# Kernel optimization log

Measured on AMD Instinct MI355X. Metric: run time of the kernel, lower is better.

The kernel has to match this reference:

```python
import jax, jax.numpy as jnp
import numpy as np

B, T, D, H, K, V, W = 2, 2048, 768, 12, 64, 64, 1024
EPS = 1e-6


def setup_inputs() -> dict:
    key = jax.random.key(0)
    ks = jax.random.split(key, 10)
    std = 0.02
    return {
        "x": jax.random.normal(ks[0], (B, T, D), jnp.float32),
        "gdn_state": jax.random.normal(ks[1], (B, H, K, V), jnp.float32),
        "Wq": jax.random.normal(ks[2], (D, H * K), jnp.float32) * std,
        "Wk": jax.random.normal(ks[3], (D, H * K), jnp.float32) * std,
        "Wv": jax.random.normal(ks[4], (D, H * K), jnp.float32) * std,
        "Wo": jax.random.normal(ks[5], (H * K, D), jnp.float32) * std,
        "Wgq": jax.random.normal(ks[6], (D, H * K), jnp.float32) * std,
        "Wro": jax.random.normal(ks[7], (H * V, D), jnp.float32) * std,
        "Wg": jax.random.normal(ks[8], (D, H), jnp.float32) * std,
        "bg": jnp.full((H,), 1.0, jnp.float32),  # swa_gate_init
        "norm_w": jnp.ones((D,), jnp.float32),
    }


def reference(x, gdn_state, Wq, Wk, Wv, Wo, Wgq, Wro, Wg, bg, norm_w):
    # RMSNorm
    xn = x * jax.lax.rsqrt(jnp.mean(x * x, axis=-1, keepdims=True) + EPS) * norm_w

    def proj(w):  # (B,T,D)@(D,HK) -> (B,H,T,K)
        return (xn @ w).reshape(B, T, H, K).transpose(0, 2, 1, 3)

    q, k, v = proj(Wq), proj(Wk), proj(Wv)
    scale = K ** -0.5

    scores = jnp.einsum("bhqk,bhsk->bhqs", q, k) * scale  # (B,H,T,T)
    i = jnp.arange(T)[:, None]
    j = jnp.arange(T)[None, :]
    allowed = (j <= i) & (j >= i - W)  # causal sliding window
    scores = jnp.where(allowed, scores, -jnp.inf)
    attn = jax.nn.softmax(scores, axis=-1)

    local = jnp.einsum("bhqs,bhsk->bhqk", attn, v)
    local = local.transpose(0, 2, 1, 3).reshape(B, T, H * K) @ Wo  # (B,T,D)

    # GDN state retrieval
    qg = jax.nn.relu((xn @ Wgq).reshape(B, T, H, K).transpose(0, 2, 1, 3))  # (B,H,T,K)
    retrieved = jnp.einsum("bhkv,bhtk->bhtv", gdn_state, qg)  # (B,H,T,V)
    retrieval = retrieved.transpose(0, 2, 1, 3).reshape(B, T, H * V) @ Wro  # (B,T,D)
    gate = jax.nn.sigmoid(xn @ Wg + bg)  # (B,T,H)
    retrieval = jnp.mean(gate, axis=-1, keepdims=True) * retrieval

    return x + local + retrieval
```

## Files before the change

kernel.cpp:

```cpp
#include <hip/hip_runtime.h>
#include <math.h>
#include <stdint.h>

typedef float f32x4 __attribute__((ext_vector_type(4)));
typedef __bf16 bf16x8 __attribute__((ext_vector_type(8)));
typedef __bf16 bf16x4 __attribute__((ext_vector_type(4)));

constexpr int Bc = 2, Tc = 2048, Dc = 768, Hc = 12, Wc = 1024;
#define CEXP 0.18033688011112042f

__device__ __forceinline__ f32x4 mfma_bf16(bf16x8 a, bf16x8 b, f32x4 c) {
    return __builtin_amdgcn_mfma_f32_16x16x32_bf16(a, b, c, 0, 0, 0);
}
__device__ __forceinline__ void gload16(const void* g, void* l) {
    __builtin_amdgcn_global_load_lds(
        (const __attribute__((address_space(1))) uint32_t*)g,
        (__attribute__((address_space(3))) uint32_t*)l, 16, 0, 0);
}
__device__ __forceinline__ uint32_t pack2(float a, float b) {
    union { __bf16 h[2]; uint32_t u; } x;
    x.h[0] = (__bf16)a; x.h[1] = (__bf16)b; return x.u;
}
__device__ __forceinline__ void s_wait_vm8()   { asm volatile("s_waitcnt vmcnt(8)" ::: "memory"); }
__device__ __forceinline__ void s_wait_vm4()   { asm volatile("s_waitcnt vmcnt(4)" ::: "memory"); }
__device__ __forceinline__ void s_wait_vm0()   { asm volatile("s_waitcnt vmcnt(0)" ::: "memory"); }
__device__ __forceinline__ void s_wait_lgkm0() { asm volatile("s_waitcnt lgkmcnt(0)" ::: "memory"); }
__device__ __forceinline__ void bar()          { __builtin_amdgcn_s_barrier(); }
__device__ __forceinline__ void wait_tiles(int infl) {
    if (infl >= 2) s_wait_vm8();
    else if (infl == 1) s_wait_vm4();
    else s_wait_vm0();
}

__global__ __launch_bounds__(256) void k_prep_w(
    const float* __restrict__ Wq, const float* __restrict__ Wk,
    const float* __restrict__ Wv, const float* __restrict__ Wgq,
    const float* __restrict__ Wo, const float* __restrict__ Wro,
    __bf16* __restrict__ wTproj, __bf16* __restrict__ wTout)
{
    __shared__ __bf16 ldsT[64][66];
    const int wsel = blockIdx.y;
    const float* srcs[6] = {Wq, Wk, Wv, Wgq, Wo, Wro};
    const float* src = srcs[wsel];
    __bf16* dst; int dstride, koff;
    if (wsel < 4) { dst = wTproj + (size_t)wsel * Dc * Dc; dstride = Dc;  koff = 0; }
    else if (wsel == 4) { dst = wTout; dstride = 1536; koff = 0; }
    else { dst = wTout; dstride = 1536; koff = 768; }
    const float scale = (wsel == 0) ? CEXP : 1.0f;

    int tile = blockIdx.x;
    int tk = tile % 12, tn = tile / 12;
    int k0 = tk * 64, n0 = tn * 64;
    int i = threadIdx.x, rsub = i >> 4, c4 = i & 15;
#pragma unroll
    for (int rep = 0; rep < 4; ++rep) {
        int row = rep * 16 + rsub;
        float4 v = *(const float4*)(src + (size_t)(k0 + row) * Dc + n0 + c4 * 4);
        ldsT[c4 * 4 + 0][row] = (__bf16)(v.x * scale);
        ldsT[c4 * 4 + 1][row] = (__bf16)(v.y * scale);
        ldsT[c4 * 4 + 2][row] = (__bf16)(v.z * scale);
        ldsT[c4 * 4 + 3][row] = (__bf16)(v.w * scale);
    }
    __syncthreads();
#pragma unroll
    for (int rep = 0; rep < 4; ++rep) {
        int n = rep * 16 + rsub;
        bf16x4 o = *(const bf16x4*)&ldsT[n][c4 * 4];
        *(bf16x4*)(dst + (size_t)(n0 + n) * dstride + koff + k0 + c4 * 4) = o;
    }
}

__global__ __launch_bounds__(256) void k_prep_state(
    const float* __restrict__ st, __bf16* __restrict__ stT)
{
    int idx = blockIdx.x * 256 + threadIdx.x;
    int bh = idx >> 12, kk = (idx >> 6) & 63, vv = idx & 63;
    stT[(size_t)bh * 4096 + vv * 64 + kk] = (__bf16)st[idx];
}

__global__ __launch_bounds__(256) void k_prep_wgt(
    const float* __restrict__ Wg, float* __restrict__ WgT)
{
    int i = blockIdx.x * 256 + threadIdx.x;
    int h = i / Dc, d = i - h * Dc;
    WgT[i] = Wg[d * 12 + h];
}

__global__ __launch_bounds__(256) void k_rmsnorm(
    const float* __restrict__ x, const float* __restrict__ norm_w,
    __bf16* __restrict__ xnb)
{
    int row = blockIdx.x, tid = threadIdx.x;
    const float* xr = x + (size_t)row * Dc;
    float4 v = make_float4(0.f, 0.f, 0.f, 0.f);
    float ss = 0.f;
    if (tid < 192) {
        v = ((const float4*)xr)[tid];
        ss = v.x * v.x + v.y * v.y + v.z * v.z + v.w * v.w;
    }
#pragma unroll
    for (int m = 32; m; m >>= 1) ss += __shfl_xor(ss, m, 64);
    __shared__ float red[4];
    if ((tid & 63) == 0) red[tid >> 6] = ss;
    __syncthreads();
    float tot = red[0] + red[1] + red[2] + red[3];
    float rms = rsqrtf(tot * (1.f / 768.f) + 1e-6f);
    if (tid < 192) {
        float4 nw = ((const float4*)norm_w)[tid];
        bf16x4 o;
        o[0] = (__bf16)(v.x * rms * nw.x);
        o[1] = (__bf16)(v.y * rms * nw.y);
        o[2] = (__bf16)(v.z * rms * nw.z);
        o[3] = (__bf16)(v.w * rms * nw.w);
        *(bf16x4*)(xnb + (size_t)row * Dc + tid * 4) = o;
    }
}

__global__ __launch_bounds__(256) void k_gate(
    const __bf16* __restrict__ xnb, const float* __restrict__ WgT,
    const float* __restrict__ bg, float* __restrict__ gmean)
{
    int row = blockIdx.x * 4 + (threadIdx.x >> 6);
    int lane = threadIdx.x & 63;
    const __bf16* xr = xnb + (size_t)row * Dc;
    float p[12];
#pragma unroll
    for (int h = 0; h < 12; ++h) p[h] = 0.f;
    for (int d = lane; d < Dc; d += 64) {
        float xv = (float)xr[d];
#pragma unroll
        for (int h = 0; h < 12; ++h) p[h] += xv * WgT[h * Dc + d];
    }
#pragma unroll
    for (int h = 0; h < 12; ++h) {
#pragma unroll
        for (int m = 32; m; m >>= 1) p[h] += __shfl_xor(p[h], m, 64);
    }
    if (lane == 0) {
        float s = 0.f;
#pragma unroll
        for (int h = 0; h < 12; ++h) s += 1.f / (1.f + expf(-(p[h] + bg[h])));
        gmean[row] = s * (1.f / 12.f);
    }
}

template <int MODE>
__global__ __launch_bounds__(256) void k_gemm(
    const __bf16* __restrict__ A, const __bf16* __restrict__ BT,
    const float* __restrict__ xres, float* __restrict__ outf,
    __bf16* __restrict__ qb, __bf16* __restrict__ kbf,
    __bf16* __restrict__ vtb, __bf16* __restrict__ qgb)
{
    constexpr int BM = (MODE == 0) ? 128 : 64;
    constexpr int BN = (MODE == 0) ? 128 : 64;
    constexpr int KD = (MODE == 0) ? 768 : 1536;
    constexpr int BK = (MODE == 0) ? 32 : 64;
    constexpr int KI = BK / 32;
    constexpr int WM = BM / 2, WN = BN / 2;
    constexpr int MI = WM / 16, NI = WN / 16;
    constexpr int MT = 4096 / BM;
    constexpr int NK = KD / BK;
    constexpr int GR = BK / 8;
    constexpr int ACH = BM * BK / 2048;
    constexpr int BCH = BN * BK / 2048;
    __shared__ __bf16 As[3][BM * BK];
    __shared__ __bf16 Bs[3][BN * BK];
    const int tid = threadIdx.x, w = tid >> 6, lane = tid & 63;
    const int g = lane >> 4, t = lane & 15;
    int id = blockIdx.x, xcd = id & 7, l = id >> 3;
    int nid = xcd * 96 + l;
    int m0 = (nid % MT) * BM, n0 = (nid / MT) * BN;
    const __bf16* Abase = A + (size_t)m0 * KD;
    const __bf16* Bbase = BT + (size_t)n0 * KD;
    const int wrow = (w >> 1) * WM, wcol = (w & 1) * WN;

    auto STAGE = [&](int buf, int k0) {
#pragma unroll
        for (int c = 0; c < ACH; ++c) {
            int chunk = c * 256 + tid, row = chunk / GR, cix = chunk % GR;
            gload16(Abase + (size_t)row * KD + k0 + cix * 8, &As[buf][chunk * 8]);
        }
#pragma unroll
        for (int c = 0; c < BCH; ++c) {
            int chunk = c * 256 + tid, row = chunk / GR, cix = chunk % GR;
            gload16(Bbase + (size_t)row * KD + k0 + cix * 8, &Bs[buf][chunk * 8]);
        }
    };

    f32x4 acc[MI][NI] = {};
    STAGE(0, 0);
    STAGE(1, BK);
    STAGE(2, 2 * BK);
    int buf = 0;
    for (int ks = 0; ks < NK; ++ks) {
        wait_tiles(NK - 1 - ks);
        bar();
        const __bf16* Ab = As[buf];
        const __bf16* Bb = Bs[buf];
        bf16x8 af[MI][KI], bfr[NI][KI];
#pragma unroll
        for (int kk = 0; kk < KI; ++kk) {
#pragma unroll
            for (int mi = 0; mi < MI; ++mi)
                af[mi][kk] = *(const bf16x8*)(Ab + (wrow + mi * 16 + t) * BK + kk * 32 + g * 8);
#pragma unroll
            for (int ni = 0; ni < NI; ++ni)
                bfr[ni][kk] = *(const bf16x8*)(Bb + (wcol + ni * 16 + t) * BK + kk * 32 + g * 8);
        }
        s_wait_lgkm0();
        __builtin_amdgcn_sched_barrier(0);
        bar();
        if (ks + 3 < NK) STAGE(buf, (ks + 3) * BK);
        buf = (buf == 2) ? 0 : buf + 1;
        __builtin_amdgcn_s_setprio(1);
#pragma unroll
        for (int kk = 0; kk < KI; ++kk)
#pragma unroll
            for (int mi = 0; mi < MI; ++mi)
#pragma unroll
                for (int ni = 0; ni < NI; ++ni)
                    acc[mi][ni] = mfma_bf16(af[mi][kk], bfr[ni][kk], acc[mi][ni]);
        __builtin_amdgcn_s_setprio(0);
    }
    const int region = (MODE == 0) ? (n0 / 768) : 0;
#pragma unroll
    for (int mi = 0; mi < MI; ++mi)
#pragma unroll
        for (int ni = 0; ni < NI; ++ni)
#pragma unroll
            for (int r = 0; r < 4; ++r) {
                int grow = m0 + wrow + mi * 16 + g * 4 + r;
                int gcol = n0 + wcol + ni * 16 + t;
                float v = acc[mi][ni][r];
                if (MODE == 1) {
                    size_t idx = (size_t)grow * Dc + gcol;
                    outf[idx] = xres[idx] + v;
                } else {
                    int c = gcol - region * 768;
                    int h = c >> 6, kd = c & 63;
                    int b = grow >> 11, ti = grow & (Tc - 1);
                    if (region == 0)
                        qb[((size_t)(b * Hc + h) * Tc + ti) * 64 + kd] = (__bf16)v;
                    else if (region == 1) {
                        int kds = kd ^ ((ti & 7) << 3);
                        kbf[((size_t)(b * Hc + h) * Tc + ti) * 64 + kds] = (__bf16)v;
                    } else if (region == 2) {
                        int kap = ti & 63;
                        int rho = (kap & 32) | (((kap >> 2) & 3) << 3) |
                                  (((kap >> 4) & 1) << 2) | (kap & 3);
                        int ts = (ti & ~63) | (rho ^ ((kd & 7) << 3));
                        vtb[((size_t)(b * Hc + h) * 64 + kd) * Tc + ts] = (__bf16)v;
                    } else
                        qgb[((size_t)(b * Hc + h) * Tc + ti) * 64 + kd] = (__bf16)fmaxf(v, 0.f);
                }
            }
}

__global__ __launch_bounds__(256) void k_attn(
    const __bf16* __restrict__ q, const __bf16* __restrict__ k,
    const __bf16* __restrict__ vt, __bf16* __restrict__ ac)
{
    __shared__ __bf16 Ks[3][64 * 64];
    __shared__ __bf16 Vs[3][64 * 64];
    int id = blockIdx.x, xcd = id & 7, l = id >> 3;
    int nid = xcd * 96 + l;
    int sblk = nid & 31, h = (nid >> 5) % Hc, b = nid / (32 * Hc);
    int tid = threadIdx.x;
    int w = tid >> 6, lane = tid & 63;
    int g = lane >> 4, t = lane & 15;
    int q0 = sblk * 64, qw = q0 + w * 16;
    const __bf16* qb = q + (size_t)(b * Hc + h) * Tc * 64;
    const __bf16* kb = k + (size_t)(b * Hc + h) * Tc * 64;
    const __bf16* vb = vt + (size_t)(b * Hc + h) * 64 * Tc;

    bf16x8 qf0 = *(const bf16x8*)(qb + (size_t)(qw + t) * 64 + g * 8);
    bf16x8 qf1 = *(const bf16x8*)(qb + (size_t)(qw + t) * 64 + 32 + g * 8);

    const int qi = qw + t;
    const int lowB = qi - Wc;
    const int xr = t & 7;

    f32x4 oacc[4] = {};
    float lsum = 0.f;

    const int s_begin = (q0 >= Wc) ? q0 - Wc : 0;
    const int NT = (q0 + 64 - s_begin) >> 6;

    auto STAGE = [&](int buf, int s0) {
#pragma unroll
        for (int j = 0; j < 2; ++j) {
            int ch = j * 256 + tid;
            gload16(kb + (size_t)(s0 + (ch >> 3)) * 64 + (ch & 7) * 8,
                    &Ks[buf][ch * 8]);
            gload16(vb + (size_t)(ch >> 3) * Tc + s0 + (ch & 7) * 8,
                    &Vs[buf][ch * 8]);
        }
    };

    STAGE(0, s_begin);
    if (NT > 1) STAGE(1, s_begin + 64);
    if (NT > 2) STAGE(2, s_begin + 128);
    int buf = 0;
    for (int it = 0; it < NT; ++it) {
        int s0 = s_begin + it * 64;
        wait_tiles(NT - 1 - it);
        bar();
        const __bf16* Kt = Ks[buf];
        const __bf16* Vt = Vs[buf];
        f32x4 sc[4];
        __builtin_amdgcn_s_setprio(1);
#pragma unroll
        for (int sub = 0; sub < 4; ++sub) {
            const __bf16* kr = Kt + (sub * 16 + t) * 64;
            bf16x8 kA = *(const bf16x8*)(kr + ((g ^ xr) << 3));
            bf16x8 kB = *(const bf16x8*)(kr + (((g + 4) ^ xr) << 3));
            f32x4 s = {};
            s = mfma_bf16(kA, qf0, s);
            s = mfma_bf16(kB, qf1, s);
            sc[sub] = s;
        }
        __builtin_amdgcn_s_setprio(0);
        float pv[4][4];
#pragma unroll
        for (int sub = 0; sub < 4; ++sub)
#pragma unroll
            for (int r = 0; r < 4; ++r) {
                int kk = s0 + sub * 16 + g * 4 + r;
                float e = exp2f(sc[sub][r]);
                float val = (kk <= qi && kk >= lowB) ? e : 0.f;
                pv[sub][r] = val;
                lsum += val;
            }
        __builtin_amdgcn_s_setprio(1);
#pragma unroll
        for (int ks = 0; ks < 2; ++ks) {
            union { uint32_t u[4]; bf16x8 v; } pf;
            pf.u[0] = pack2(pv[ks * 2][0], pv[ks * 2][1]);
            pf.u[1] = pack2(pv[ks * 2][2], pv[ks * 2][3]);
            pf.u[2] = pack2(pv[ks * 2 + 1][0], pv[ks * 2 + 1][1]);
            pf.u[3] = pack2(pv[ks * 2 + 1][2], pv[ks * 2 + 1][3]);
#pragma unroll
            for (int n = 0; n < 4; ++n) {
                const __bf16* vrow = Vt + (n * 16 + t) * 64;
                bf16x8 vf = *(const bf16x8*)(vrow + ((((ks * 4) + g) ^ xr) << 3));
                oacc[n] = mfma_bf16(pf.v, vf, oacc[n]);
            }
        }
        __builtin_amdgcn_s_setprio(0);
        s_wait_lgkm0();
        __builtin_amdgcn_sched_barrier(0);
        bar();
        if (it + 3 < NT) STAGE(buf, s0 + 192);
        buf = (buf == 2) ? 0 : buf + 1;
    }
    lsum += __shfl_xor(lsum, 16, 64);
    lsum += __shfl_xor(lsum, 32, 64);
    float linv = 1.f / lsum;
    float lq[4];
#pragma unroll
    for (int r = 0; r < 4; ++r) lq[r] = __shfl(linv, g * 4 + r, 64);
#pragma unroll
    for (int n = 0; n < 4; ++n)
#pragma unroll
        for (int r = 0; r < 4; ++r) {
            int qrow = qw + g * 4 + r;
            ac[(size_t)(b * Tc + qrow) * 1536 + h * 64 + n * 16 + t] =
                (__bf16)(oacc[n][r] * lq[r]);
        }
}

__global__ __launch_bounds__(256) void k_retr(
    const __bf16* __restrict__ qg, const __bf16* __restrict__ stateT,
    const float* __restrict__ gmean, __bf16* __restrict__ ac)
{
    int b = blockIdx.z, h = blockIdx.y;
    int w = threadIdx.x >> 6, lane = threadIdx.x & 63;
    int g = lane >> 4, t = lane & 15;
    int t0 = blockIdx.x * 64 + w * 16;
    const __bf16* qbp = qg + (size_t)(b * Hc + h) * Tc * 64;
    const __bf16* sb = stateT + (size_t)(b * Hc + h) * 64 * 64;
    bf16x8 a0 = *(const bf16x8*)(qbp + (size_t)(t0 + t) * 64 + g * 8);
    bf16x8 a1 = *(const bf16x8*)(qbp + (size_t)(t0 + t) * 64 + 32 + g * 8);
#pragma unroll
    for (int n = 0; n < 4; ++n) {
        bf16x8 b0 = *(const bf16x8*)(sb + (n * 16 + t) * 64 + g * 8);
        bf16x8 b1 = *(const bf16x8*)(sb + (n * 16 + t) * 64 + 32 + g * 8);
        f32x4 acc = {};
        acc = mfma_bf16(a0, b0, acc);
        acc = mfma_bf16(a1, b1, acc);
#pragma unroll
        for (int r = 0; r < 4; ++r) {
            int ti = t0 + g * 4 + r;
            float gm = gmean[b * Tc + ti];
            ac[(size_t)(b * Tc + ti) * 1536 + 768 + h * 64 + n * 16 + t] =
                (__bf16)(acc[r] * gm);
        }
    }
}

extern "C" void kernel_launch(void* const* d_in, const int* in_sizes, int n_in,
                              void* d_out, int out_size, void* d_ws, size_t ws_size,
                              hipStream_t stream) {
    (void)in_sizes; (void)n_in; (void)out_size; (void)ws_size;
    const float* x     = (const float*)d_in[0];
    const float* gdn   = (const float*)d_in[1];
    const float* Wq    = (const float*)d_in[2];
    const float* Wk    = (const float*)d_in[3];
    const float* Wv    = (const float*)d_in[4];
    const float* Wo    = (const float*)d_in[5];
    const float* Wgq   = (const float*)d_in[6];
    const float* Wro   = (const float*)d_in[7];
    const float* Wg    = (const float*)d_in[8];
    const float* bg    = (const float*)d_in[9];
    const float* normw = (const float*)d_in[10];
    float* out = (float*)d_out;

    char* p = (char*)d_ws;
    auto alloc = [&](size_t bytes) -> char* {
        char* r = p; p += (bytes + 255) & ~(size_t)255; return r;
    };
    constexpr size_t NROW = (size_t)Bc * Tc;
    __bf16* xnb    = (__bf16*)alloc(NROW * Dc * 2);
    __bf16* wTproj = (__bf16*)alloc((size_t)4 * Dc * Dc * 2);
    __bf16* wTout  = (__bf16*)alloc((size_t)Dc * 1536 * 2);
    __bf16* stT    = (__bf16*)alloc((size_t)Bc * Hc * 64 * 64 * 2);
    __bf16* qbuf   = (__bf16*)alloc(NROW * Dc * 2);
    __bf16* kbuf   = (__bf16*)alloc(NROW * Dc * 2);
    __bf16* qgbuf  = (__bf16*)alloc(NROW * Dc * 2);
    __bf16* vtbuf  = (__bf16*)alloc(NROW * Dc * 2);
    __bf16* ac     = (__bf16*)alloc(NROW * 1536 * 2);
    float*  gmean  = (float*)alloc(NROW * 4);
    float*  WgT    = (float*)alloc((size_t)12 * Dc * 4);

    k_prep_w<<<dim3(144, 6), 256, 0, stream>>>(Wq, Wk, Wv, Wgq, Wo, Wro, wTproj, wTout);
    k_prep_state<<<(Bc * Hc * 64 * 64) / 256, 256, 0, stream>>>(gdn, stT);
    k_prep_wgt<<<36, 256, 0, stream>>>(Wg, WgT);
    k_rmsnorm<<<NROW, 256, 0, stream>>>(x, normw, xnb);
    k_gate<<<NROW / 4, 256, 0, stream>>>(xnb, WgT, bg, gmean);

    k_gemm<0><<<768, 256, 0, stream>>>(xnb, wTproj, nullptr, nullptr,
                                       qbuf, kbuf, vtbuf, qgbuf);
    k_attn<<<768, 256, 0, stream>>>(qbuf, kbuf, vtbuf, ac);
    k_retr<<<dim3(Tc / 64, Hc, Bc), 256, 0, stream>>>(qgbuf, stT, gmean, ac);
    k_gemm<1><<<768, 256, 0, stream>>>(ac, wTout, x, out,
                                       nullptr, nullptr, nullptr, nullptr);
}
```

Baseline: 138.0 us.

## Split attention key tiles across two wave groups, fuse retrieval, double-buffer GEMM

The attention kernel now runs 512 threads. Two groups of four waves take alternating key tiles for the same query rows, and their partial outputs and row sums are combined through LDS at the end. This roughly halves the serial loop length per wave while adding a reduction step and more register pressure. The separate retrieval kernel is folded into the attention epilogue to save a launch, and the GEMM pipeline drops from triple to double buffering to cut LDS use, at the risk of exposing more load latency.

Result: faster. 129.8 us (-5.9%).

```diff
diff --git a/kernel.cpp b/kernel.cpp
--- a/kernel.cpp
+++ b/kernel.cpp
@@ -21,14 +21,14 @@
     union { __bf16 h[2]; uint32_t u; } x;
     x.h[0] = (__bf16)a; x.h[1] = (__bf16)b; return x.u;
 }
-__device__ __forceinline__ void s_wait_vm8()   { asm volatile("s_waitcnt vmcnt(8)" ::: "memory"); }
 __device__ __forceinline__ void s_wait_vm4()   { asm volatile("s_waitcnt vmcnt(4)" ::: "memory"); }
+__device__ __forceinline__ void s_wait_vm2()   { asm volatile("s_waitcnt vmcnt(2)" ::: "memory"); }
 __device__ __forceinline__ void s_wait_vm0()   { asm volatile("s_waitcnt vmcnt(0)" ::: "memory"); }
 __device__ __forceinline__ void s_wait_lgkm0() { asm volatile("s_waitcnt lgkmcnt(0)" ::: "memory"); }
 __device__ __forceinline__ void bar()          { __builtin_amdgcn_s_barrier(); }
-__device__ __forceinline__ void wait_tiles(int infl) {
-    if (infl >= 2) s_wait_vm8();
-    else if (infl == 1) s_wait_vm4();
+__device__ __forceinline__ void wait_tiles2(int infl) {
+    if (infl >= 2) s_wait_vm4();
+    else if (infl == 1) s_wait_vm2();
     else s_wait_vm0();
 }
 
@@ -163,8 +163,8 @@
     constexpr int GR = BK / 8;
     constexpr int ACH = BM * BK / 2048;
     constexpr int BCH = BN * BK / 2048;
-    __shared__ __bf16 As[3][BM * BK];
-    __shared__ __bf16 Bs[3][BN * BK];
+    __shared__ __bf16 As[2][BM * BK];
+    __shared__ __bf16 Bs[2][BN * BK];
     const int tid = threadIdx.x, w = tid >> 6, lane = tid & 63;
     const int g = lane >> 4, t = lane & 15;
     int id = blockIdx.x, xcd = id & 7, l = id >> 3;
@@ -190,13 +190,11 @@
     f32x4 acc[MI][NI] = {};
     STAGE(0, 0);
     STAGE(1, BK);
-    STAGE(2, 2 * BK);
-    int buf = 0;
     for (int ks = 0; ks < NK; ++ks) {
-        wait_tiles(NK - 1 - ks);
+        if (ks == NK - 1) s_wait_vm0(); else s_wait_vm4();
         bar();
-        const __bf16* Ab = As[buf];
-        const __bf16* Bb = Bs[buf];
+        const __bf16* Ab = As[ks & 1];
+        const __bf16* Bb = Bs[ks & 1];
         bf16x8 af[MI][KI], bfr[NI][KI];
 #pragma unroll
         for (int kk = 0; kk < KI; ++kk) {
@@ -210,8 +208,7 @@
         s_wait_lgkm0();
         __builtin_amdgcn_sched_barrier(0);
         bar();
-        if (ks + 3 < NK) STAGE(buf, (ks + 3) * BK);
-        buf = (buf == 2) ? 0 : buf + 1;
+        if (ks + 2 < NK) STAGE(ks & 1, (ks + 2) * BK);
         __builtin_amdgcn_s_setprio(1);
 #pragma unroll
         for (int kk = 0; kk < KI; ++kk)
@@ -256,9 +253,11 @@
             }
 }
 
-__global__ __launch_bounds__(256) void k_attn(
+__global__ __launch_bounds__(512, 6) void k_attn(
     const __bf16* __restrict__ q, const __bf16* __restrict__ k,
-    const __bf16* __restrict__ vt, __bf16* __restrict__ ac)
+    const __bf16* __restrict__ vt, const __bf16* __restrict__ qg,
+    const __bf16* __restrict__ stateT, const float* __restrict__ gmean,
+    __bf16* __restrict__ ac)
 {
     __shared__ __bf16 Ks[3][64 * 64];
     __shared__ __bf16 Vs[3][64 * 64];
@@ -268,7 +267,8 @@
     int tid = threadIdx.x;
     int w = tid >> 6, lane = tid & 63;
     int g = lane >> 4, t = lane & 15;
-    int q0 = sblk * 64, qw = q0 + w * 16;
+    int q0 = sblk * 64, qw = q0 + (w & 3) * 16;
+    const int myPar = w >> 2;
     const __bf16* qb = q + (size_t)(b * Hc + h) * Tc * 64;
     const __bf16* kb = k + (size_t)(b * Hc + h) * Tc * 64;
     const __bf16* vb = vt + (size_t)(b * Hc + h) * 64 * Tc;
@@ -287,14 +287,9 @@
     const int NT = (q0 + 64 - s_begin) >> 6;
 
     auto STAGE = [&](int buf, int s0) {
-#pragma unroll
-        for (int j = 0; j < 2; ++j) {
-            int ch = j * 256 + tid;
-            gload16(kb + (size_t)(s0 + (ch >> 3)) * 64 + (ch & 7) * 8,
-                    &Ks[buf][ch * 8]);
-            gload16(vb + (size_t)(ch >> 3) * Tc + s0 + (ch & 7) * 8,
-                    &Vs[buf][ch * 8]);
-        }
+        int ch = tid;
+        gload16(kb + (size_t)(s0 + (ch >> 3)) * 64 + (ch & 7) * 8, &Ks[buf][ch * 8]);
+        gload16(vb + (size_t)(ch >> 3) * Tc + s0 + (ch & 7) * 8, &Vs[buf][ch * 8]);
     };
 
     STAGE(0, s_begin);
@@ -303,97 +298,103 @@
     int buf = 0;
     for (int it = 0; it < NT; ++it) {
         int s0 = s_begin + it * 64;
-        wait_tiles(NT - 1 - it);
+        wait_tiles2(NT - 1 - it);
         bar();
-        const __bf16* Kt = Ks[buf];
-        const __bf16* Vt = Vs[buf];
-        f32x4 sc[4];
-        __builtin_amdgcn_s_setprio(1);
-#pragma unroll
-        for (int sub = 0; sub < 4; ++sub) {
-            const __bf16* kr = Kt + (sub * 16 + t) * 64;
-            bf16x8 kA = *(const bf16x8*)(kr + ((g ^ xr) << 3));
-            bf16x8 kB = *(const bf16x8*)(kr + (((g + 4) ^ xr) << 3));
-            f32x4 s = {};
-            s = mfma_bf16(kA, qf0, s);
-            s = mfma_bf16(kB, qf1, s);
-            sc[sub] = s;
+        if ((it & 1) == myPar) {
+            const __bf16* Kt = Ks[buf];
+            const __bf16* Vt = Vs[buf];
+            f32x4 sc[4];
+            __builtin_amdgcn_s_setprio(1);
+#pragma unroll
+            for (int sub = 0; sub < 4; ++sub) {
+                const __bf16* kr = Kt + (sub * 16 + t) * 64;
+                bf16x8 kA = *(const bf16x8*)(kr + ((g ^ xr) << 3));
+                bf16x8 kB = *(const bf16x8*)(kr + (((g + 4) ^ xr) << 3));
+                f32x4 s = {};
+                s = mfma_bf16(kA, qf0, s);
+                s = mfma_bf16(kB, qf1, s);
+                sc[sub] = s;
+            }
+            __builtin_amdgcn_s_setprio(0);
+            float pv[4][4];
+#pragma unroll
+            for (int sub = 0; sub < 4; ++sub)
+#pragma unroll
+                for (int r = 0; r < 4; ++r) {
+                    int kk = s0 + sub * 16 + g * 4 + r;
+                    float e = exp2f(sc[sub][r]);
+                    float val = (kk <= qi && kk >= lowB) ? e : 0.f;
+                    pv[sub][r] = val;
+                    lsum += val;
+                }
+            __builtin_amdgcn_s_setprio(1);
+#pragma unroll
+            for (int ks = 0; ks < 2; ++ks) {
+                union { uint32_t u[4]; bf16x8 v; } pf;
+                pf.u[0] = pack2(pv[ks * 2][0], pv[ks * 2][1]);
+                pf.u[1] = pack2(pv[ks * 2][2], pv[ks * 2][3]);
+                pf.u[2] = pack2(pv[ks * 2 + 1][0], pv[ks * 2 + 1][1]);
+                pf.u[3] = pack2(pv[ks * 2 + 1][2], pv[ks * 2 + 1][3]);
+#pragma unroll
+                for (int n = 0; n < 4; ++n) {
+                    const __bf16* vrow = Vt + (n * 16 + t) * 64;
+                    bf16x8 vf = *(const bf16x8*)(vrow + ((((ks * 4) + g) ^ xr) << 3));
+                    oacc[n] = mfma_bf16(pf.v, vf, oacc[n]);
+                }
+            }
+            __builtin_amdgcn_s_setprio(0);
         }
-        __builtin_amdgcn_s_setprio(0);
-        float pv[4][4];
-#pragma unroll
-        for (int sub = 0; sub < 4; ++sub)
-#pragma unroll
-            for (int r = 0; r < 4; ++r) {
-                int kk = s0 + sub * 16 + g * 4 + r;
-                float e = exp2f(sc[sub][r]);
-                float val = (kk <= qi && kk >= lowB) ? e : 0.f;
-                pv[sub][r] = val;
-                lsum += val;
-            }
-        __builtin_amdgcn_s_setprio(1);
-#pragma unroll
-        for (int ks = 0; ks < 2; ++ks) {
-            union { uint32_t u[4]; bf16x8 v; } pf;
-            pf.u[0] = pack2(pv[ks * 2][0], pv[ks * 2][1]);
-            pf.u[1] = pack2(pv[ks * 2][2], pv[ks * 2][3]);
-            pf.u[2] = pack2(pv[ks * 2 + 1][0], pv[ks * 2 + 1][1]);
-            pf.u[3] = pack2(pv[ks * 2 + 1][2], pv[ks * 2 + 1][3]);
-#pragma unroll
-            for (int n = 0; n < 4; ++n) {
-                const __bf16* vrow = Vt + (n * 16 + t) * 64;
-                bf16x8 vf = *(const bf16x8*)(vrow + ((((ks * 4) + g) ^ xr) << 3));
-                oacc[n] = mfma_bf16(pf.v, vf, oacc[n]);
-            }
-        }
-        __builtin_amdgcn_s_setprio(0);
         s_wait_lgkm0();
         __builtin_amdgcn_sched_barrier(0);
         bar();
         if (it + 3 < NT) STAGE(buf, s0 + 192);
         buf = (buf == 2) ? 0 : buf + 1;
     }
-    lsum += __shfl_xor(lsum, 16, 64);
-    lsum += __shfl_xor(lsum, 32, 64);
-    float linv = 1.f / lsum;
-    float lq[4];
-#pragma unroll
-    for (int r = 0; r < 4; ++r) lq[r] = __shfl(linv, g * 4 + r, 64);
-#pragma unroll
-    for (int n = 0; n < 4; ++n)
-#pragma unroll
-        for (int r = 0; r < 4; ++r) {
-            int qrow = qw + g * 4 + r;
-            ac[(size_t)(b * Tc + qrow) * 1536 + h * 64 + n * 16 + t] =
-                (__bf16)(oacc[n][r] * lq[r]);
-        }
-}
-
-__global__ __launch_bounds__(256) void k_retr(
-    const __bf16* __restrict__ qg, const __bf16* __restrict__ stateT,
-    const float* __restrict__ gmean, __bf16* __restrict__ ac)
-{
-    int b = blockIdx.z, h = blockIdx.y;
-    int w = threadIdx.x >> 6, lane = threadIdx.x & 63;
-    int g = lane >> 4, t = lane & 15;
-    int t0 = blockIdx.x * 64 + w * 16;
-    const __bf16* qbp = qg + (size_t)(b * Hc + h) * Tc * 64;
-    const __bf16* sb = stateT + (size_t)(b * Hc + h) * 64 * 64;
-    bf16x8 a0 = *(const bf16x8*)(qbp + (size_t)(t0 + t) * 64 + g * 8);
-    bf16x8 a1 = *(const bf16x8*)(qbp + (size_t)(t0 + t) * 64 + 32 + g * 8);
-#pragma unroll
-    for (int n = 0; n < 4; ++n) {
-        bf16x8 b0 = *(const bf16x8*)(sb + (n * 16 + t) * 64 + g * 8);
-        bf16x8 b1 = *(const bf16x8*)(sb + (n * 16 + t) * 64 + 32 + g * 8);
-        f32x4 acc = {};
-        acc = mfma_bf16(a0, b0, acc);
-        acc = mfma_bf16(a1, b1, acc);
-#pragma unroll
-        for (int r = 0; r < 4; ++r) {
-            int ti = t0 + g * 4 + r;
-            float gm = gmean[b * Tc + ti];
-            ac[(size_t)(b * Tc + ti) * 1536 + 768 + h * 64 + n * 16 + t] =
-                (__bf16)(acc[r] * gm);
+    float* cb = (float*)&Ks[0][0];
+    if (w >= 4) {
+        float* dst = cb + ((size_t)((w - 4) * 64 + lane)) * 20;
+#pragma unroll
+        for (int n = 0; n < 4; ++n) *(f32x4*)(dst + n * 4) = oacc[n];
+        dst[16] = lsum;
+    }
+    bar();
+    if (w < 4) {
+        const float* src = cb + ((size_t)(w * 64 + lane)) * 20;
+#pragma unroll
+        for (int n = 0; n < 4; ++n) oacc[n] += *(const f32x4*)(src + n * 4);
+        lsum += src[16];
+        lsum += __shfl_xor(lsum, 16, 64);
+        lsum += __shfl_xor(lsum, 32, 64);
+        float linv = 1.f / lsum;
+        float lq[4];
+#pragma unroll
+        for (int r = 0; r < 4; ++r) lq[r] = __shfl(linv, g * 4 + r, 64);
+#pragma unroll
+        for (int n = 0; n < 4; ++n)
+#pragma unroll
+            for (int r = 0; r < 4; ++r) {
+                int qrow = qw + g * 4 + r;
+                ac[(size_t)(b * Tc + qrow) * 1536 + h * 64 + n * 16 + t] =
+                    (__bf16)(oacc[n][r] * lq[r]);
+            }
+        const __bf16* qgp = qg + (size_t)(b * Hc + h) * Tc * 64;
+        const __bf16* sb = stateT + (size_t)(b * Hc + h) * 4096;
+        bf16x8 a0 = *(const bf16x8*)(qgp + (size_t)(qw + t) * 64 + g * 8);
+        bf16x8 a1 = *(const bf16x8*)(qgp + (size_t)(qw + t) * 64 + 32 + g * 8);
+#pragma unroll
+        for (int n = 0; n < 4; ++n) {
+            bf16x8 b0 = *(const bf16x8*)(sb + (n * 16 + t) * 64 + g * 8);
+            bf16x8 b1 = *(const bf16x8*)(sb + (n * 16 + t) * 64 + 32 + g * 8);
+            f32x4 acc2 = {};
+            acc2 = mfma_bf16(a0, b0, acc2);
+            acc2 = mfma_bf16(a1, b1, acc2);
+#pragma unroll
+            for (int r = 0; r < 4; ++r) {
+                int ti = qw + g * 4 + r;
+                float gm = gmean[b * Tc + ti];
+                ac[(size_t)(b * Tc + ti) * 1536 + 768 + h * 64 + n * 16 + t] =
+                    (__bf16)(acc2[r] * gm);
+            }
         }
     }
 }
@@ -440,8 +441,7 @@
 
     k_gemm<0><<<768, 256, 0, stream>>>(xnb, wTproj, nullptr, nullptr,
                                        qbuf, kbuf, vtbuf, qgbuf);
-    k_attn<<<768, 256, 0, stream>>>(qbuf, kbuf, vtbuf, ac);
-    k_retr<<<dim3(Tc / 64, Hc, Bc), 256, 0, stream>>>(qgbuf, stT, gmean, ac);
+    k_attn<<<768, 512, 0, stream>>>(qbuf, kbuf, vtbuf, qgbuf, stT, gmean, ac);
     k_gemm<1><<<768, 256, 0, stream>>>(ac, wTout, x, out,
                                        nullptr, nullptr, nullptr, nullptr);
 }
```
